# Kernel tuning notes

Hardware: AMD Instinct MI355X
Metric: run time of the kernel (lower is better)

Reference implementation:

```python
import jax, jax.numpy as jnp
import numpy as np

B, N, G, D = 16, 4096, 1024, 256
NUM_STEPS = 4
DT = 0.01
EPS = 1e-5


def _layernorm(x, g, b):
    mu = jnp.mean(x, axis=-1, keepdims=True)
    var = jnp.var(x, axis=-1, keepdims=True)
    return (x - mu) * jax.lax.rsqrt(var + EPS) * g + b


def setup_inputs() -> dict:
    key = jax.random.key(0)
    ks = jax.random.split(key, 6)
    embeddings = jax.random.normal(ks[0], (B, N, D), dtype=jnp.float32)
    positions = jax.random.uniform(ks[1], (B, N, 1), dtype=jnp.float32)
    grid_points = jnp.broadcast_to(jnp.linspace(0.0, 1.0, G, dtype=jnp.float32)[None, :, None], (B, G, 1))
    sigma = jnp.asarray(0.2, dtype=jnp.float32)          # RBF bandwidth
    alpha = jnp.asarray(0.1, dtype=jnp.float32)          # diffusion coefficient
    W_int = jax.random.normal(ks[2], (D, D), dtype=jnp.float32) * 0.02  # interference mixing
    b_int = jnp.zeros((D,), dtype=jnp.float32)
    W_out = jax.random.normal(ks[3], (D, D), dtype=jnp.float32) * 0.02  # output_proj
    b_out = jnp.zeros((D,), dtype=jnp.float32)
    ln1_g = jnp.ones((D,), dtype=jnp.float32)
    ln1_b = jnp.zeros((D,), dtype=jnp.float32)
    ln2_g = jnp.ones((D,), dtype=jnp.float32)
    ln2_b = jnp.zeros((D,), dtype=jnp.float32)
    return {"embeddings": embeddings, "positions": positions, "grid_points": grid_points,
            "sigma": sigma, "alpha": alpha, "W_int": W_int, "b_int": b_int,
            "W_out": W_out, "b_out": b_out, "ln1_g": ln1_g, "ln1_b": ln1_b,
            "ln2_g": ln2_g, "ln2_b": ln2_b}


def reference(embeddings, positions, grid_points, sigma, alpha, W_int, b_int,
              W_out, b_out, ln1_g, ln1_b, ln2_g, ln2_b):
    # --- FieldProjector: RBF kernel-weighted token -> grid projection ---
    # dist2: [B, N, G]
    dist2 = jnp.sum((positions[:, :, None, :] - grid_points[:, None, :, :]) ** 2, axis=-1)
    kern = jnp.exp(-dist2 / (2.0 * sigma * sigma))
    field = jnp.einsum('bng,bnd->bgd', kern, embeddings)  # [B, G, D]

    # --- UnifiedFieldDynamics: multi-step diffusion + standard interference ---
    for _ in range(NUM_STEPS):
        padded = jnp.pad(field, ((0, 0), (1, 1), (0, 0)), mode='edge')
        lap = padded[:, 2:] - 2.0 * field + padded[:, :-2]          # 1D grid Laplacian
        interference = jnp.tanh(jnp.einsum('bgd,de->bge', field, W_int) + b_int)
        field = field + DT * (alpha * lap + interference)

    # --- FieldSampler: linear interpolation grid -> token positions ---
    u = positions[..., 0] * (G - 1)                                  # continuous grid index [B, N]
    i0 = jnp.clip(jnp.floor(u), 0, G - 2).astype(jnp.int32)
    w = (u - i0.astype(u.dtype))[..., None]                          # [B, N, 1]
    f0 = jnp.take_along_axis(field, i0[..., None], axis=1)           # [B, N, D]
    f1 = jnp.take_along_axis(field, (i0 + 1)[..., None], axis=1)
    sampled = (1.0 - w) * f0 + w * f1

    # --- Residual + LayerNorm + Linear epilogue ---
    enhanced = _layernorm(sampled + embeddings, ln1_g, ln1_b)
    out = jnp.einsum('bnd,de->bne', enhanced, W_out) + b_out         # dropout is identity (p=0)
    out = _layernorm(out + enhanced, ln2_g, ln2_b)
    return out
```

## Files before the change

### kernel.cpp

```cpp
#include <hip/hip_runtime.h>
#include <math.h>

#define B_ 16
#define N_ 4096
#define G_ 1024
#define D_ 256
#define DT_ 0.01f
#define EPS_ 1e-5f

typedef float f32x4 __attribute__((ext_vector_type(4)));
typedef short bf16x8 __attribute__((ext_vector_type(8)));
typedef unsigned short u16;

__device__ __forceinline__ float fast_tanh(float x) {
    float e = __expf(2.0f * x);
    return 1.0f - __fdividef(2.0f, e + 1.0f);
}

__device__ __forceinline__ u16 f2b(float x) {
    unsigned u = __float_as_uint(x);
    unsigned r = (u + 0x7FFFu + ((u >> 16) & 1u)) >> 16;
    return (u16)r;
}
__device__ __forceinline__ float b2f(u16 h) {
    return __uint_as_float(((unsigned)h) << 16);
}

__device__ __forceinline__ void split_pack8(const float f[8], uint4& vh, uint4& vl) {
    u16 h[8], l[8];
#pragma unroll
    for (int j = 0; j < 8; ++j) {
        h[j] = f2b(f[j]);
        l[j] = f2b(f[j] - b2f(h[j]));
    }
    vh = make_uint4((unsigned)h[0] | ((unsigned)h[1] << 16), (unsigned)h[2] | ((unsigned)h[3] << 16),
                    (unsigned)h[4] | ((unsigned)h[5] << 16), (unsigned)h[6] | ((unsigned)h[7] << 16));
    vl = make_uint4((unsigned)l[0] | ((unsigned)l[1] << 16), (unsigned)l[2] | ((unsigned)l[3] << 16),
                    (unsigned)l[4] | ((unsigned)l[5] << 16), (unsigned)l[6] | ((unsigned)l[7] << 16));
}

__device__ __forceinline__ void split8(const float f[8], bf16x8& h8, bf16x8& l8) {
    union { uint4 u; bf16x8 v; } H, L;
    split_pack8(f, H.u, L.u);
    h8 = H.v; l8 = L.v;
}


__global__ __launch_bounds__(256) void k_wsplit(const float* __restrict__ Wi,
                                                const float* __restrict__ Wo,
                                                u16* __restrict__ wbase) {
    const float* W = blockIdx.y ? Wo : Wi;
    u16* Th = wbase + (size_t)blockIdx.y * 131072;
    u16* Tl = Th + 65536;
    int e0 = (blockIdx.x * 256 + threadIdx.x) * 2;
#pragma unroll
    for (int i = 0; i < 2; ++i) {
        int e = e0 + i;
        int c = e >> 8, k = e & 255;
        float v = W[(size_t)k * D_ + c];
        u16 h = f2b(v);
        Th[e] = h;
        Tl[e] = f2b(v - b2f(h));
    }
}

__global__ __launch_bounds__(256) void k_esplit(const float* __restrict__ emb,
                                                u16* __restrict__ Eh,
                                                u16* __restrict__ El) {
    __shared__ float sT[64][68];
    const int t  = threadIdx.x;
    const int b  = blockIdx.z;
    const int n0 = blockIdx.y * 64;
    const int d0 = blockIdx.x * 64;
    const float* Eb = emb + (size_t)b * N_ * D_;

#pragma unroll
    for (int s = 0; s < 4; ++s) {
        int fi  = t + 256 * s;
        int row = fi >> 4;
        int c4  = (fi & 15) * 4;
        float4 v = *(const float4*)&Eb[(size_t)(n0 + row) * D_ + d0 + c4];
        *(float4*)&sT[row][c4] = v;
    }
    __syncthreads();

    const int d  = t >> 2;
    const int ng = t & 3;
    u16 h[16], l[16];
#pragma unroll
    for (int i = 0; i < 16; ++i) {
        float v = sT[ng * 16 + i][d];
        h[i] = f2b(v);
        l[i] = f2b(v - b2f(h[i]));
    }
    size_t ob = ((size_t)b * D_ + d0 + d) * N_ + n0 + ng * 16;
    uint4 H0 = make_uint4((unsigned)h[0] | ((unsigned)h[1] << 16), (unsigned)h[2] | ((unsigned)h[3] << 16),
                          (unsigned)h[4] | ((unsigned)h[5] << 16), (unsigned)h[6] | ((unsigned)h[7] << 16));
    uint4 H1 = make_uint4((unsigned)h[8] | ((unsigned)h[9] << 16), (unsigned)h[10] | ((unsigned)h[11] << 16),
                          (unsigned)h[12] | ((unsigned)h[13] << 16), (unsigned)h[14] | ((unsigned)h[15] << 16));
    uint4 L0 = make_uint4((unsigned)l[0] | ((unsigned)l[1] << 16), (unsigned)l[2] | ((unsigned)l[3] << 16),
                          (unsigned)l[4] | ((unsigned)l[5] << 16), (unsigned)l[6] | ((unsigned)l[7] << 16));
    uint4 L1 = make_uint4((unsigned)l[8] | ((unsigned)l[9] << 16), (unsigned)l[10] | ((unsigned)l[11] << 16),
                          (unsigned)l[12] | ((unsigned)l[13] << 16), (unsigned)l[14] | ((unsigned)l[15] << 16));
    *(uint4*)&Eh[ob]     = H0;
    *(uint4*)&Eh[ob + 8] = H1;
    *(uint4*)&El[ob]     = L0;
    *(uint4*)&El[ob + 8] = L1;
}

__global__ __launch_bounds__(256, 2) void k_proj_a(const u16* __restrict__ Eh,
                                                   const u16* __restrict__ El,
                                                   const float* __restrict__ pos,
                                                   const float* __restrict__ grd,
                                                   const float* __restrict__ sigma_p,
                                                   float* __restrict__ field) {
    __shared__ u16 sKh[64][40], sKl[64][40];

    const int t    = threadIdx.x;
    const int lane = t & 63;
    const int w    = t >> 6;
    const int wg   = w & 1;
    const int wd   = w >> 1;
    const int q    = lane >> 4;
    const int r16  = lane & 15;

    const int bt = blockIdx.z;
    const int g0 = blockIdx.y * 64;
    const int d0 = blockIdx.x * 128;

    const float sg = sigma_p[0];
    const float inv2s2 = 1.0f / (2.0f * sg * sg);
    const float* Pb = pos + (size_t)bt * N_;

    const int kg = t >> 2;
    const int k8 = (t & 3) * 8;
    const float xg = grd[(size_t)bt * G_ + g0 + kg];

    const u16* Ehb = Eh + (size_t)bt * D_ * N_;
    const u16* Elb = El + (size_t)bt * D_ * N_;
    size_t cb[4];
#pragma unroll
    for (int n = 0; n < 4; ++n)
        cb[n] = (size_t)(d0 + wd * 64 + n * 16 + r16) * N_ + q * 8;

    f32x4 acc[2][4];
#pragma unroll
    for (int m = 0; m < 2; ++m)
#pragma unroll
        for (int n = 0; n < 4; ++n) acc[m][n] = (f32x4){0.f, 0.f, 0.f, 0.f};

    for (int n0 = 0; n0 < N_; n0 += 32) {
        bf16x8 bh[4], bl[4];
#pragma unroll
        for (int n = 0; n < 4; ++n) {
            bh[n] = *(const bf16x8*)&Ehb[cb[n] + n0];
            bl[n] = *(const bf16x8*)&Elb[cb[n] + n0];
        }
        float4 p0 = *(const float4*)&Pb[n0 + k8];
        float4 p1 = *(const float4*)&Pb[n0 + k8 + 4];
        float pv[8] = {p0.x, p0.y, p0.z, p0.w, p1.x, p1.y, p1.z, p1.w};
        float kv[8];
#pragma unroll
        for (int j = 0; j < 8; ++j) {
            float dx = pv[j] - xg;
            kv[j] = __expf(-dx * dx * inv2s2);
        }

        __syncthreads();
        {
            uint4 vh, vl;
            split_pack8(kv, vh, vl);
            *(uint4*)&sKh[kg][k8] = vh;
            *(uint4*)&sKl[kg][k8] = vl;
        }
        __syncthreads();

        bf16x8 ah[2], al_[2];
#pragma unroll
        for (int m = 0; m < 2; ++m) {
            int row = wg * 32 + m * 16 + r16;
            ah[m]  = *(const bf16x8*)&sKh[row][q * 8];
            al_[m] = *(const bf16x8*)&sKl[row][q * 8];
        }
#pragma unroll
        for (int n = 0; n < 4; ++n)
#pragma unroll
            for (int m = 0; m < 2; ++m) {
                f32x4 c = acc[m][n];
                c = __builtin_amdgcn_mfma_f32_16x16x32_bf16(al_[m], bh[n], c, 0, 0, 0);
                c = __builtin_amdgcn_mfma_f32_16x16x32_bf16(ah[m], bl[n], c, 0, 0, 0);
                c = __builtin_amdgcn_mfma_f32_16x16x32_bf16(ah[m], bh[n], c, 0, 0, 0);
                acc[m][n] = c;
            }
    }

#pragma unroll
    for (int m = 0; m < 2; ++m) {
        int gr = g0 + wg * 32 + m * 16 + q * 4;
#pragma unroll
        for (int n = 0; n < 4; ++n) {
            int dc = d0 + wd * 64 + n * 16 + r16;
            f32x4 c = acc[m][n];
#pragma unroll
            for (int r = 0; r < 4; ++r)
                field[((size_t)bt * G_ + gr + r) * D_ + dc] = c[r];
        }
    }
}

__global__ __launch_bounds__(256, 2) void k_diff_a(const float* __restrict__ fin,
                                                   float* __restrict__ fout,
                                                   const u16* __restrict__ Wh,
                                                   const u16* __restrict__ Wl,
                                                   const float* __restrict__ bint,
                                                   const float* __restrict__ alpha_p) {
    const int t    = threadIdx.x;
    const int lane = t & 63;
    const int w    = t >> 6;
    const int wg   = w & 1;
    const int wd   = w >> 1;
    const int q    = lane >> 4;
    const int r16  = lane & 15;

    const int r0 = blockIdx.y * 64;
    const int c0 = blockIdx.x * 128;

    size_t arow[2], cb[4];
#pragma unroll
    for (int m = 0; m < 2; ++m)
        arow[m] = (size_t)(r0 + wg * 32 + m * 16 + r16) * D_ + q * 8;
#pragma unroll
    for (int n = 0; n < 4; ++n)
        cb[n] = (size_t)(c0 + wd * 64 + n * 16 + r16) * D_ + q * 8;

    f32x4 acc[2][4];
#pragma unroll
    for (int m = 0; m < 2; ++m)
#pragma unroll
        for (int n = 0; n < 4; ++n) acc[m][n] = (f32x4){0.f, 0.f, 0.f, 0.f};

    for (int k0 = 0; k0 < D_; k0 += 32) {
        bf16x8 ah[2], al_[2];
#pragma unroll
        for (int m = 0; m < 2; ++m) {
            float4 a0 = *(const float4*)&fin[arow[m] + k0];
            float4 a1 = *(const float4*)&fin[arow[m] + k0 + 4];
            float fa[8] = {a0.x, a0.y, a0.z, a0.w, a1.x, a1.y, a1.z, a1.w};
            split8(fa, ah[m], al_[m]);
        }
#pragma unroll
        for (int n = 0; n < 4; ++n) {
            bf16x8 bh = *(const bf16x8*)&Wh[cb[n] + k0];
            bf16x8 bl = *(const bf16x8*)&Wl[cb[n] + k0];
#pragma unroll
            for (int m = 0; m < 2; ++m) {
                f32x4 c = acc[m][n];
                c = __builtin_amdgcn_mfma_f32_16x16x32_bf16(al_[m], bh, c, 0, 0, 0);
                c = __builtin_amdgcn_mfma_f32_16x16x32_bf16(ah[m], bl, c, 0, 0, 0);
                c = __builtin_amdgcn_mfma_f32_16x16x32_bf16(ah[m], bh, c, 0, 0, 0);
                acc[m][n] = c;
            }
        }
    }

    const float al = alpha_p[0];
#pragma unroll
    for (int m = 0; m < 2; ++m) {
#pragma unroll
        for (int n = 0; n < 4; ++n) {
            const int dc = c0 + wd * 64 + n * 16 + r16;
            const float bi = bint[dc];
            f32x4 c = acc[m][n];
#pragma unroll
            for (int r = 0; r < 4; ++r) {
                const int row = r0 + wg * 32 + m * 16 + q * 4 + r;
                const int g = row & (G_ - 1);
                const float fc = fin[(size_t)row * D_ + dc];
                const float fu = fin[(size_t)(g == 0 ? row : row - 1) * D_ + dc];
                const float fd = fin[(size_t)(g == G_ - 1 ? row : row + 1) * D_ + dc];
                const float y  = fast_tanh(c[r] + bi);
                fout[(size_t)row * D_ + dc] = fc + DT_ * (al * (fu + fd - 2.0f * fc) + y);
            }
        }
    }
}

__global__ __launch_bounds__(256, 2) void k_out_a(const float* __restrict__ enh,
                                                  const u16* __restrict__ Wh,
                                                  const u16* __restrict__ Wl,
                                                  const float* __restrict__ bo,
                                                  const float* __restrict__ g2,
                                                  const float* __restrict__ b2,
                                                  float* __restrict__ out) {
    __shared__ float sO[32][260];

    const int t    = threadIdx.x;
    const int lane = t & 63;
    const int w    = t >> 6;
    const int wg   = w & 1;
    const int wd   = w >> 1;
    const int q    = lane >> 4;
    const int r16  = lane & 15;

    const int r0 = blockIdx.x * 32;

    size_t arow = (size_t)(r0 + wg * 16 + r16) * D_ + q * 8;
    size_t cb[8];
#pragma unroll
    for (int n = 0; n < 8; ++n)
        cb[n] = (size_t)(wd * 128 + n * 16 + r16) * D_ + q * 8;

    f32x4 acc[8];
#pragma unroll
    for (int n = 0; n < 8; ++n) acc[n] = (f32x4){0.f, 0.f, 0.f, 0.f};

    for (int k0 = 0; k0 < D_; k0 += 32) {
        float4 a0 = *(const float4*)&enh[arow + k0];
        float4 a1 = *(const float4*)&enh[arow + k0 + 4];
        float fa[8] = {a0.x, a0.y, a0.z, a0.w, a1.x, a1.y, a1.z, a1.w};
        bf16x8 ah, al_;
        split8(fa, ah, al_);
#pragma unroll
        for (int n = 0; n < 8; ++n) {
            bf16x8 bh = *(const bf16x8*)&Wh[cb[n] + k0];
            bf16x8 bl = *(const bf16x8*)&Wl[cb[n] + k0];
            f32x4 c = acc[n];
            c = __builtin_amdgcn_mfma_f32_16x16x32_bf16(al_, bh, c, 0, 0, 0);
            c = __builtin_amdgcn_mfma_f32_16x16x32_bf16(ah, bl, c, 0, 0, 0);
            c = __builtin_amdgcn_mfma_f32_16x16x32_bf16(ah, bh, c, 0, 0, 0);
            acc[n] = c;
        }
    }

#pragma unroll
    for (int n = 0; n < 8; ++n)
#pragma unroll
        for (int r = 0; r < 4; ++r)
            sO[wg * 16 + q * 4 + r][wd * 128 + n * 16 + r16] = acc[n][r];
    __syncthreads();

    const int er = t >> 3;
    const int ec = (t & 7) * 32;
    const size_t grow = (size_t)(r0 + er) * D_;

    float y[32];
    float s1 = 0.f, s2 = 0.f;
#pragma unroll
    for (int j = 0; j < 8; ++j) {
        float4 a  = *(const float4*)&sO[er][ec + j * 4];
        float4 bv = *(const float4*)&bo[ec + j * 4];
        float4 e  = *(const float4*)&enh[grow + ec + j * 4];
        float v0 = a.x + bv.x + e.x, v1 = a.y + bv.y + e.y;
        float v2 = a.z + bv.z + e.z, v3 = a.w + bv.w + e.w;
        y[j * 4 + 0] = v0; y[j * 4 + 1] = v1; y[j * 4 + 2] = v2; y[j * 4 + 3] = v3;
        s1 += v0 + v1 + v2 + v3;
        s2 += v0 * v0 + v1 * v1 + v2 * v2 + v3 * v3;
    }
#pragma unroll
    for (int m = 1; m < 8; m <<= 1) {
        s1 += __shfl_xor(s1, m);
        s2 += __shfl_xor(s2, m);
    }
    float mu  = s1 * (1.0f / 256.0f);
    float var = s2 * (1.0f / 256.0f) - mu * mu;
    float rs  = rsqrtf(var + EPS_);
#pragma unroll
    for (int j = 0; j < 8; ++j) {
        float4 gv  = *(const float4*)&g2[ec + j * 4];
        float4 b2v = *(const float4*)&b2[ec + j * 4];
        float4 o;
        o.x = (y[j * 4 + 0] - mu) * rs * gv.x + b2v.x;
        o.y = (y[j * 4 + 1] - mu) * rs * gv.y + b2v.y;
        o.z = (y[j * 4 + 2] - mu) * rs * gv.z + b2v.z;
        o.w = (y[j * 4 + 3] - mu) * rs * gv.w + b2v.w;
        *(float4*)&out[grow + ec + j * 4] = o;
    }
}

__global__ __launch_bounds__(256) void k_sample(const float* __restrict__ field,
                                                const float* __restrict__ emb,
                                                const float* __restrict__ pos,
                                                const float* __restrict__ g1,
                                                const float* __restrict__ b1,
                                                float* __restrict__ enh) {
    const int row  = blockIdx.x * 4 + (threadIdx.x >> 6);
    const int lane = threadIdx.x & 63;
    const int b    = row >> 12;
    const int d    = lane * 4;

    float p  = pos[row];
    float u  = p * (float)(G_ - 1);
    float fi = floorf(u);
    fi = fminf(fmaxf(fi, 0.0f), (float)(G_ - 2));
    int   i0 = (int)fi;
    float ww = u - fi;

    const float4 f0v = *(const float4*)&field[((size_t)(b << 10) + i0) * D_ + d];
    const float4 f1v = *(const float4*)&field[((size_t)(b << 10) + i0 + 1) * D_ + d];
    const float4 ev  = *(const float4*)&emb[(size_t)row * D_ + d];

    float y[4];
    y[0] = f0v.x + ww * (f1v.x - f0v.x) + ev.x;
    y[1] = f0v.y + ww * (f1v.y - f0v.y) + ev.y;
    y[2] = f0v.z + ww * (f1v.z - f0v.z) + ev.z;
    y[3] = f0v.w + ww * (f1v.w - f0v.w) + ev.w;

    float s1 = y[0] + y[1] + y[2] + y[3];
    float s2 = y[0]*y[0] + y[1]*y[1] + y[2]*y[2] + y[3]*y[3];
#pragma unroll
    for (int m = 1; m < 64; m <<= 1) {
        s1 += __shfl_xor(s1, m);
        s2 += __shfl_xor(s2, m);
    }
    float mu  = s1 * (1.0f / 256.0f);
    float var = s2 * (1.0f / 256.0f) - mu * mu;
    float rs  = rsqrtf(var + EPS_);

    const float4 gv = *(const float4*)&g1[d];
    const float4 bv = *(const float4*)&b1[d];
    float4 o;
    o.x = (y[0] - mu) * rs * gv.x + bv.x;
    o.y = (y[1] - mu) * rs * gv.y + bv.y;
    o.z = (y[2] - mu) * rs * gv.z + bv.z;
    o.w = (y[3] - mu) * rs * gv.w + bv.w;
    *(float4*)&enh[(size_t)row * D_ + d] = o;
}

__global__ __launch_bounds__(256, 2) void k_proj_b(const float* __restrict__ emb,
                                                   const float* __restrict__ pos,
                                                   const float* __restrict__ grd,
                                                   const float* __restrict__ sigma_p,
                                                   float* __restrict__ field) {
    __shared__ u16 sKh[64][40], sKl[64][40];
    __shared__ u16 sEh[128][40], sEl[128][40];

    const int t = threadIdx.x, lane = t & 63, w = t >> 6;
    const int wg = w & 1, wd = w >> 1, q = lane >> 4, r16 = lane & 15;
    const int bt = blockIdx.z, g0 = blockIdx.y * 64, d0 = blockIdx.x * 128;
    const float sg = sigma_p[0], inv2s2 = 1.0f / (2.0f * sg * sg);
    const float* Eb = emb + (size_t)bt * N_ * D_;
    const float* Pb = pos + (size_t)bt * N_;
    const int kg = t >> 2, k8 = (t & 3) * 8;
    const float xg = grd[(size_t)bt * G_ + g0 + kg];
    const int ek = t >> 5, ed = (t & 31) * 4;

    f32x4 acc[2][4];
#pragma unroll
    for (int m = 0; m < 2; ++m)
#pragma unroll
        for (int n = 0; n < 4; ++n) acc[m][n] = (f32x4){0.f, 0.f, 0.f, 0.f};

    for (int n0 = 0; n0 < N_; n0 += 32) {
        float4 ev[4];
#pragma unroll
        for (int s = 0; s < 4; ++s)
            ev[s] = *(const float4*)&Eb[(size_t)(n0 + ek + 8 * s) * D_ + d0 + ed];
        float kv[8];
#pragma unroll
        for (int j = 0; j < 8; ++j) {
            float p = Pb[n0 + k8 + j];
            float dx = p - xg;
            kv[j] = __expf(-dx * dx * inv2s2);
        }
        __syncthreads();
        {
            uint4 vh, vl;
            split_pack8(kv, vh, vl);
            *(uint4*)&sKh[kg][k8] = vh;
            *(uint4*)&sKl[kg][k8] = vl;
        }
#pragma unroll
        for (int s = 0; s < 4; ++s) {
            int kk = ek + 8 * s;
            float f[4] = {ev[s].x, ev[s].y, ev[s].z, ev[s].w};
#pragma unroll
            for (int i = 0; i < 4; ++i) {
                u16 h = f2b(f[i]);
                sEh[ed + i][kk] = h;
                sEl[ed + i][kk] = f2b(f[i] - b2f(h));
            }
        }
        __syncthreads();
        bf16x8 ah[2], al_[2];
#pragma unroll
        for (int m = 0; m < 2; ++m) {
            int row = wg * 32 + m * 16 + r16;
            ah[m]  = *(const bf16x8*)&sKh[row][q * 8];
            al_[m] = *(const bf16x8*)&sKl[row][q * 8];
        }
#pragma unroll
        for (int n = 0; n < 4; ++n) {
            int row = wd * 64 + n * 16 + r16;
            bf16x8 bh = *(const bf16x8*)&sEh[row][q * 8];
            bf16x8 bl = *(const bf16x8*)&sEl[row][q * 8];
#pragma unroll
            for (int m = 0; m < 2; ++m) {
                f32x4 c = acc[m][n];
                c = __builtin_amdgcn_mfma_f32_16x16x32_bf16(al_[m], bh, c, 0, 0, 0);
                c = __builtin_amdgcn_mfma_f32_16x16x32_bf16(ah[m], bl, c, 0, 0, 0);
                c = __builtin_amdgcn_mfma_f32_16x16x32_bf16(ah[m], bh, c, 0, 0, 0);
                acc[m][n] = c;
            }
        }
    }
#pragma unroll
    for (int m = 0; m < 2; ++m) {
        int gr = g0 + wg * 32 + m * 16 + q * 4;
#pragma unroll
        for (int n = 0; n < 4; ++n) {
            int dc = d0 + wd * 64 + n * 16 + r16;
            f32x4 c = acc[m][n];
#pragma unroll
            for (int r = 0; r < 4; ++r)
                field[((size_t)bt * G_ + gr + r) * D_ + dc] = c[r];
        }
    }
}

__global__ __launch_bounds__(256, 2) void k_diff_b(const float* __restrict__ fin,
                                                   float* __restrict__ fout,
                                                   const float* __restrict__ W,
                                                   const float* __restrict__ bint,
                                                   const float* __restrict__ alpha_p) {
    __shared__ u16 sAh[64][40], sAl[64][40];
    __shared__ u16 sWh[128][40], sWl[128][40];

    const int t = threadIdx.x, lane = t & 63, w = t >> 6;
    const int wg = w & 1, wd = w >> 1, q = lane >> 4, r16 = lane & 15;
    const int r0 = blockIdx.y * 64, c0 = blockIdx.x * 128;
    const int ar = t >> 2, ak = (t & 3) * 8, ek = t >> 5, ed = (t & 31) * 4;

    f32x4 acc[2][4];
#pragma unroll
    for (int m = 0; m < 2; ++m)
#pragma unroll
        for (int n = 0; n < 4; ++n) acc[m][n] = (f32x4){0.f, 0.f, 0.f, 0.f};

    for (int k0 = 0; k0 < D_; k0 += 32) {
        float4 a0 = *(const float4*)&fin[(size_t)(r0 + ar) * D_ + k0 + ak];
        float4 a1 = *(const float4*)&fin[(size_t)(r0 + ar) * D_ + k0 + ak + 4];
        float4 wv[4];
#pragma unroll
        for (int s = 0; s < 4; ++s)
            wv[s] = *(const float4*)&W[(size_t)(k0 + ek + 8 * s) * D_ + c0 + ed];
        __syncthreads();
        {
            float fa[8] = {a0.x, a0.y, a0.z, a0.w, a1.x, a1.y, a1.z, a1.w};
            uint4 vh, vl;
            split_pack8(fa, vh, vl);
            *(uint4*)&sAh[ar][ak] = vh;
            *(uint4*)&sAl[ar][ak] = vl;
        }
#pragma unroll
        for (int s = 0; s < 4; ++s) {
            int kk = ek + 8 * s;
            float f[4] = {wv[s].x, wv[s].y, wv[s].z, wv[s].w};
#pragma unroll
            for (int i = 0; i < 4; ++i) {
                u16 h = f2b(f[i]);
                sWh[ed + i][kk] = h;
                sWl[ed + i][kk] = f2b(f[i] - b2f(h));
            }
        }
        __syncthreads();
        bf16x8 ah[2], al_[2];
#pragma unroll
        for (int m = 0; m < 2; ++m) {
            int row = wg * 32 + m * 16 + r16;
            ah[m]  = *(const bf16x8*)&sAh[row][q * 8];
            al_[m] = *(const bf16x8*)&sAl[row][q * 8];
        }
#pragma unroll
        for (int n = 0; n < 4; ++n) {
            int col = wd * 64 + n * 16 + r16;
            bf16x8 bh = *(const bf16x8*)&sWh[col][q * 8];
            bf16x8 bl = *(const bf16x8*)&sWl[col][q * 8];
#pragma unroll
            for (int m = 0; m < 2; ++m) {
                f32x4 c = acc[m][n];
                c = __builtin_amdgcn_mfma_f32_16x16x32_bf16(al_[m], bh, c, 0, 0, 0);
                c = __builtin_amdgcn_mfma_f32_16x16x32_bf16(ah[m], bl, c, 0, 0, 0);
                c = __builtin_amdgcn_mfma_f32_16x16x32_bf16(ah[m], bh, c, 0, 0, 0);
                acc[m][n] = c;
            }
        }
    }

    const float al = alpha_p[0];
#pragma unroll
    for (int m = 0; m < 2; ++m) {
#pragma unroll
        for (int n = 0; n < 4; ++n) {
            const int dc = c0 + wd * 64 + n * 16 + r16;
            const float bi = bint[dc];
            f32x4 c = acc[m][n];
#pragma unroll
            for (int r = 0; r < 4; ++r) {
                const int row = r0 + wg * 32 + m * 16 + q * 4 + r;
                const int g = row & (G_ - 1);
                const float fc = fin[(size_t)row * D_ + dc];
                const float fu = fin[(size_t)(g == 0 ? row : row - 1) * D_ + dc];
                const float fd = fin[(size_t)(g == G_ - 1 ? row : row + 1) * D_ + dc];
                const float y  = fast_tanh(c[r] + bi);
                fout[(size_t)row * D_ + dc] = fc + DT_ * (al * (fu + fd - 2.0f * fc) + y);
            }
        }
    }
}

__global__ __launch_bounds__(256, 2) void k_out_b(const float* __restrict__ enh,
                                                  const float* __restrict__ W,
                                                  const float* __restrict__ bo,
                                                  const float* __restrict__ g2,
                                                  const float* __restrict__ b2,
                                                  float* __restrict__ out) {
    __shared__ __align__(16) char smem[46080];
    u16 (*sAh)[40] = (u16(*)[40])(smem);
    u16 (*sAl)[40] = (u16(*)[40])(smem + 2560);
    u16 (*sWh)[40] = (u16(*)[40])(smem + 5120);
    u16 (*sWl)[40] = (u16(*)[40])(smem + 25600);
    float (*sO)[260] = (float(*)[260])(smem);

    const int t = threadIdx.x, lane = t & 63, w = t >> 6;
    const int wg = w & 1, wd = w >> 1, q = lane >> 4, r16 = lane & 15;
    const int r0 = blockIdx.x * 32;
    const int arow = t >> 3, akq = (t & 7) * 4, wk = t >> 6, wed = (t & 63) * 4;

    f32x4 acc[8];
#pragma unroll
    for (int n = 0; n < 8; ++n) acc[n] = (f32x4){0.f, 0.f, 0.f, 0.f};

    for (int k0 = 0; k0 < D_; k0 += 32) {
        float4 av = *(const float4*)&enh[(size_t)(r0 + arow) * D_ + k0 + akq];
        float4 wv[8];
#pragma unroll
        for (int s = 0; s < 8; ++s)
            wv[s] = *(const float4*)&W[(size_t)(k0 + wk + 4 * s) * D_ + wed];
        __syncthreads();
        {
            float fa[4] = {av.x, av.y, av.z, av.w};
            u16 h[4], l[4];
#pragma unroll
            for (int j = 0; j < 4; ++j) {
                h[j] = f2b(fa[j]);
                l[j] = f2b(fa[j] - b2f(h[j]));
            }
            *(uint2*)&sAh[arow][akq] = make_uint2((unsigned)h[0] | ((unsigned)h[1] << 16),
                                                  (unsigned)h[2] | ((unsigned)h[3] << 16));
            *(uint2*)&sAl[arow][akq] = make_uint2((unsigned)l[0] | ((unsigned)l[1] << 16),
                                                  (unsigned)l[2] | ((unsigned)l[3] << 16));
        }
#pragma unroll
        for (int s = 0; s < 8; ++s) {
            int kk = wk + 4 * s;
            float f[4] = {wv[s].x, wv[s].y, wv[s].z, wv[s].w};
#pragma unroll
            for (int i = 0; i < 4; ++i) {
                u16 h = f2b(f[i]);
                sWh[wed + i][kk] = h;
                sWl[wed + i][kk] = f2b(f[i] - b2f(h));
            }
        }
        __syncthreads();
        bf16x8 ah  = *(const bf16x8*)&sAh[wg * 16 + r16][q * 8];
        bf16x8 al_ = *(const bf16x8*)&sAl[wg * 16 + r16][q * 8];
#pragma unroll
        for (int n = 0; n < 8; ++n) {
            int col = wd * 128 + n * 16 + r16;
            bf16x8 bh = *(const bf16x8*)&sWh[col][q * 8];
            bf16x8 bl = *(const bf16x8*)&sWl[col][q * 8];
            f32x4 c = acc[n];
            c = __builtin_amdgcn_mfma_f32_16x16x32_bf16(al_, bh, c, 0, 0, 0);
            c = __builtin_amdgcn_mfma_f32_16x16x32_bf16(ah, bl, c, 0, 0, 0);
            c = __builtin_amdgcn_mfma_f32_16x16x32_bf16(ah, bh, c, 0, 0, 0);
            acc[n] = c;
        }
    }

    __syncthreads();
#pragma unroll
    for (int n = 0; n < 8; ++n)
#pragma unroll
        for (int r = 0; r < 4; ++r)
            sO[wg * 16 + q * 4 + r][wd * 128 + n * 16 + r16] = acc[n][r];
    __syncthreads();

    const int er = t >> 3;
    const int ec = (t & 7) * 32;
    const size_t grow = (size_t)(r0 + er) * D_;

    float y[32];
    float s1 = 0.f, s2 = 0.f;
#pragma unroll
    for (int j = 0; j < 8; ++j) {
        float4 a  = *(const float4*)&sO[er][ec + j * 4];
        float4 bv = *(const float4*)&bo[ec + j * 4];
        float4 e  = *(const float4*)&enh[grow + ec + j * 4];
        float v0 = a.x + bv.x + e.x, v1 = a.y + bv.y + e.y;
        float v2 = a.z + bv.z + e.z, v3 = a.w + bv.w + e.w;
        y[j * 4 + 0] = v0; y[j * 4 + 1] = v1; y[j * 4 + 2] = v2; y[j * 4 + 3] = v3;
        s1 += v0 + v1 + v2 + v3;
        s2 += v0 * v0 + v1 * v1 + v2 * v2 + v3 * v3;
    }
#pragma unroll
    for (int m = 1; m < 8; m <<= 1) {
        s1 += __shfl_xor(s1, m);
        s2 += __shfl_xor(s2, m);
    }
    float mu  = s1 * (1.0f / 256.0f);
    float var = s2 * (1.0f / 256.0f) - mu * mu;
    float rs  = rsqrtf(var + EPS_);
#pragma unroll
    for (int j = 0; j < 8; ++j) {
        float4 gv  = *(const float4*)&g2[ec + j * 4];
        float4 b2v = *(const float4*)&b2[ec + j * 4];
        float4 o;
        o.x = (y[j * 4 + 0] - mu) * rs * gv.x + b2v.x;
        o.y = (y[j * 4 + 1] - mu) * rs * gv.y + b2v.y;
        o.z = (y[j * 4 + 2] - mu) * rs * gv.z + b2v.z;
        o.w = (y[j * 4 + 3] - mu) * rs * gv.w + b2v.w;
        *(float4*)&out[grow + ec + j * 4] = o;
    }
}

extern "C" void kernel_launch(void* const* d_in, const int* in_sizes, int n_in,
                              void* d_out, int out_size, void* d_ws, size_t ws_size,
                              hipStream_t stream) {
    const float* emb   = (const float*)d_in[0];
    const float* pos   = (const float*)d_in[1];
    const float* grd   = (const float*)d_in[2];
    const float* sigma = (const float*)d_in[3];
    const float* alpha = (const float*)d_in[4];
    const float* W_int = (const float*)d_in[5];
    const float* b_int = (const float*)d_in[6];
    const float* W_out = (const float*)d_in[7];
    const float* b_out = (const float*)d_in[8];
    const float* g1    = (const float*)d_in[9];
    const float* b1    = (const float*)d_in[10];
    const float* g2    = (const float*)d_in[11];
    const float* b2    = (const float*)d_in[12];
    float* out = (float*)d_out;

    const size_t W_BYTES  = 524288;
    const size_t F_BYTES  = (size_t)B_ * G_ * D_ * 4;
    const size_t E_BYTES  = (size_t)B_ * D_ * N_ * 2;
    const size_t NEED = W_BYTES + 2 * F_BYTES + 2 * E_BYTES;

    if (ws_size >= NEED) {
        char* ws = (char*)d_ws;
        u16*   Wih = (u16*)ws;
        u16*   Wil = Wih + 65536;
        u16*   Woh = Wih + 131072;
        u16*   Wol = Wih + 196608;
        float* f0  = (float*)(ws + W_BYTES);
        float* f1  = (float*)(ws + W_BYTES + F_BYTES);
        u16*   Eh  = (u16*)(ws + W_BYTES + 2 * F_BYTES);
        u16*   El  = (u16*)(ws + W_BYTES + 2 * F_BYTES + E_BYTES);

        k_wsplit<<<dim3(128, 2), 256, 0, stream>>>(W_int, W_out, Wih);
        k_esplit<<<dim3(4, 64, 16), 256, 0, stream>>>(emb, Eh, El);
        k_proj_a<<<dim3(2, 16, 16), 256, 0, stream>>>(Eh, El, pos, grd, sigma, f0);
        k_diff_a<<<dim3(2, 256), 256, 0, stream>>>(f0, f1, Wih, Wil, b_int, alpha);
        k_diff_a<<<dim3(2, 256), 256, 0, stream>>>(f1, f0, Wih, Wil, b_int, alpha);
        k_diff_a<<<dim3(2, 256), 256, 0, stream>>>(f0, f1, Wih, Wil, b_int, alpha);
        k_diff_a<<<dim3(2, 256), 256, 0, stream>>>(f1, f0, Wih, Wil, b_int, alpha);
        k_sample<<<(B_ * N_) / 4, 256, 0, stream>>>(f0, emb, pos, g1, b1, out);
        k_out_a<<<(B_ * N_) / 32, 256, 0, stream>>>(out, Woh, Wol, b_out, g2, b2, out);
    } else {
        float* f0 = (float*)d_ws;
        float* f1 = f0 + (size_t)B_ * G_ * D_;
        k_proj_b<<<dim3(2, 16, 16), 256, 0, stream>>>(emb, pos, grd, sigma, f0);
        k_diff_b<<<dim3(2, 256), 256, 0, stream>>>(f0, f1, W_int, b_int, alpha);
        k_diff_b<<<dim3(2, 256), 256, 0, stream>>>(f1, f0, W_int, b_int, alpha);
        k_diff_b<<<dim3(2, 256), 256, 0, stream>>>(f0, f1, W_int, b_int, alpha);
        k_diff_b<<<dim3(2, 256), 256, 0, stream>>>(f1, f0, W_int, b_int, alpha);
        k_sample<<<(B_ * N_) / 4, 256, 0, stream>>>(f0, emb, pos, g1, b1, out);
        k_out_b<<<(B_ * N_) / 32, 256, 0, stream>>>(out, W_out, b_out, g2, b2, out);
    }
}
```

Baseline: 704.1 us.

## Split-K the RBF projection, compute kernel weights in registers, add reduction pass

```diff
diff --git a/kernel.cpp b/kernel.cpp
--- a/kernel.cpp
+++ b/kernel.cpp
@@ -1,4 +1,5 @@
 #include <hip/hip_runtime.h>
+#include <hip/hip_bf16.h>
 #include <math.h>
 
 #define B_ 16
@@ -108,84 +109,78 @@
     *(uint4*)&El[ob + 8] = L1;
 }
 
-__global__ __launch_bounds__(256, 2) void k_proj_a(const u16* __restrict__ Eh,
+__global__ __launch_bounds__(256, 2) void k_proj_c(const u16* __restrict__ Eh,
                                                    const u16* __restrict__ El,
                                                    const float* __restrict__ pos,
                                                    const float* __restrict__ grd,
                                                    const float* __restrict__ sigma_p,
-                                                   float* __restrict__ field) {
-    __shared__ u16 sKh[64][40], sKl[64][40];
-
+                                                   float* __restrict__ P0,
+                                                   float* __restrict__ P1,
+                                                   float* __restrict__ P2,
+                                                   float* __restrict__ P3) {
     const int t    = threadIdx.x;
     const int lane = t & 63;
     const int w    = t >> 6;
-    const int wg   = w & 1;
-    const int wd   = w >> 1;
     const int q    = lane >> 4;
     const int r16  = lane & 15;
 
-    const int bt = blockIdx.z;
-    const int g0 = blockIdx.y * 64;
-    const int d0 = blockIdx.x * 128;
-
-    const float sg = sigma_p[0];
-    const float inv2s2 = 1.0f / (2.0f * sg * sg);
-    const float* Pb = pos + (size_t)bt * N_;
-
-    const int kg = t >> 2;
-    const int k8 = (t & 3) * 8;
-    const float xg = grd[(size_t)bt * G_ + g0 + kg];
+    const int d0 = blockIdx.x * 64;
+    const int g0 = blockIdx.y * 256 + w * 64;
+    const int bt = blockIdx.z >> 2;
+    const int ks = blockIdx.z & 3;
+
+    float* dst = (ks == 0) ? P0 : (ks == 1) ? P1 : (ks == 2) ? P2 : P3;
+
+    const float sg   = sigma_p[0];
+    const float negc = -1.0f / (2.0f * sg * sg);
+    const float* Pb  = pos + (size_t)bt * N_;
+
+    float xs[4];
+#pragma unroll
+    for (int m = 0; m < 4; ++m)
+        xs[m] = grd[(size_t)bt * G_ + g0 + m * 16 + r16];
 
     const u16* Ehb = Eh + (size_t)bt * D_ * N_;
     const u16* Elb = El + (size_t)bt * D_ * N_;
-    size_t cb[4];
+    unsigned cb[4];
 #pragma unroll
     for (int n = 0; n < 4; ++n)
-        cb[n] = (size_t)(d0 + wd * 64 + n * 16 + r16) * N_ + q * 8;
-
-    f32x4 acc[2][4];
-#pragma unroll
-    for (int m = 0; m < 2; ++m)
+        cb[n] = (unsigned)((d0 + n * 16 + r16) * N_ + ks * 1024 + q * 8);
+
+    f32x4 acc[4][4];
+#pragma unroll
+    for (int m = 0; m < 4; ++m)
 #pragma unroll
         for (int n = 0; n < 4; ++n) acc[m][n] = (f32x4){0.f, 0.f, 0.f, 0.f};
 
-    for (int n0 = 0; n0 < N_; n0 += 32) {
+    const int kbase = ks * 1024;
+    for (int kk = 0; kk < 1024; kk += 32) {
         bf16x8 bh[4], bl[4];
 #pragma unroll
         for (int n = 0; n < 4; ++n) {
-            bh[n] = *(const bf16x8*)&Ehb[cb[n] + n0];
-            bl[n] = *(const bf16x8*)&Elb[cb[n] + n0];
-        }
-        float4 p0 = *(const float4*)&Pb[n0 + k8];
-        float4 p1 = *(const float4*)&Pb[n0 + k8 + 4];
+            bh[n] = *(const bf16x8*)&Ehb[cb[n] + kk];
+            bl[n] = *(const bf16x8*)&Elb[cb[n] + kk];
+        }
+        float4 p0 = *(const float4*)&Pb[kbase + kk + q * 8];
+        float4 p1 = *(const float4*)&Pb[kbase + kk + q * 8 + 4];
         float pv[8] = {p0.x, p0.y, p0.z, p0.w, p1.x, p1.y, p1.z, p1.w};
-        float kv[8];
-#pragma unroll
-        for (int j = 0; j < 8; ++j) {
-            float dx = pv[j] - xg;
-            kv[j] = __expf(-dx * dx * inv2s2);
-        }
-
-        __syncthreads();
-        {
-            uint4 vh, vl;
-            split_pack8(kv, vh, vl);
-            *(uint4*)&sKh[kg][k8] = vh;
-            *(uint4*)&sKl[kg][k8] = vl;
-        }
-        __syncthreads();
-
-        bf16x8 ah[2], al_[2];
-#pragma unroll
-        for (int m = 0; m < 2; ++m) {
-            int row = wg * 32 + m * 16 + r16;
-            ah[m]  = *(const bf16x8*)&sKh[row][q * 8];
-            al_[m] = *(const bf16x8*)&sKl[row][q * 8];
-        }
+
+        bf16x8 ah[4], al_[4];
+#pragma unroll
+        for (int m = 0; m < 4; ++m) {
+            float ev[8];
+#pragma unroll
+            for (int j = 0; j < 8; ++j) {
+                float dx = pv[j] - xs[m];
+                ev[j] = __expf(dx * dx * negc);
+            }
+            split8(ev, ah[m], al_[m]);
+        }
+
 #pragma unroll
         for (int n = 0; n < 4; ++n)
 #pragma unroll
-            for (int m = 0; m < 2; ++m) {
+            for (int m = 0; m < 4; ++m) {
                 f32x4 c = acc[m][n];
                 c = __builtin_amdgcn_mfma_f32_16x16x32_bf16(al_[m], bh[n], c, 0, 0, 0);
                 c = __builtin_amdgcn_mfma_f32_16x16x32_bf16(ah[m], bl[n], c, 0, 0, 0);
@@ -195,16 +190,37 @@
     }
 
 #pragma unroll
-    for (int m = 0; m < 2; ++m) {
-        int gr = g0 + wg * 32 + m * 16 + q * 4;
+    for (int m = 0; m < 4; ++m) {
+        int gr = g0 + m * 16 + q * 4;
 #pragma unroll
         for (int n = 0; n < 4; ++n) {
-            int dc = d0 + wd * 64 + n * 16 + r16;
+            int dc = d0 + n * 16 + r16;
             f32x4 c = acc[m][n];
 #pragma unroll
             for (int r = 0; r < 4; ++r)
-                field[((size_t)bt * G_ + gr + r) * D_ + dc] = c[r];
-        }
+                dst[((size_t)bt * G_ + gr + r) * D_ + dc] = c[r];
+        }
+    }
+}
+
+__global__ __launch_bounds__(256) void k_kadd(float* __restrict__ P0,
+                                              const float* __restrict__ P1,
+                                              const float* __restrict__ P2,
+                                              const float* __restrict__ P3) {
+    const int i = blockIdx.x * 256 + threadIdx.x;
+    const int STRIDE = 262144;
+#pragma unroll
+    for (int k = 0; k < 4; ++k) {
+        int idx = i + k * STRIDE;
+        float4 a = *(const float4*)&P0[idx * 4];
+        float4 b = *(const float4*)&P1[idx * 4];
+        float4 c = *(const float4*)&P2[idx * 4];
+        float4 d = *(const float4*)&P3[idx * 4];
+        a.x += b.x + c.x + d.x;
+        a.y += b.y + c.y + d.y;
+        a.z += b.z + c.z + d.z;
+        a.w += b.w + c.w + d.w;
+        *(float4*)&P0[idx * 4] = a;
     }
 }
 
@@ -756,10 +772,13 @@
         float* f1  = (float*)(ws + W_BYTES + F_BYTES);
         u16*   Eh  = (u16*)(ws + W_BYTES + 2 * F_BYTES);
         u16*   El  = (u16*)(ws + W_BYTES + 2 * F_BYTES + E_BYTES);
+        float* p2  = out;
+        float* p3  = out + (size_t)B_ * G_ * D_;
 
         k_wsplit<<<dim3(128, 2), 256, 0, stream>>>(W_int, W_out, Wih);
         k_esplit<<<dim3(4, 64, 16), 256, 0, stream>>>(emb, Eh, El);
-        k_proj_a<<<dim3(2, 16, 16), 256, 0, stream>>>(Eh, El, pos, grd, sigma, f0);
+        k_proj_c<<<dim3(4, 4, 64), 256, 0, stream>>>(Eh, El, pos, grd, sigma, f0, f1, p2, p3);
+        k_kadd<<<1024, 256, 0, stream>>>(f0, f1, p2, p3);
         k_diff_a<<<dim3(2, 256), 256, 0, stream>>>(f0, f1, Wih, Wil, b_int, alpha);
         k_diff_a<<<dim3(2, 256), 256, 0, stream>>>(f1, f0, Wih, Wil, b_int, alpha);
         k_diff_a<<<dim3(2, 256), 256, 0, stream>>>(f0, f1, Wih, Wil, b_int, alpha);
```

After: 648.4 us. 1.09x faster.
